# Kernel optimization log

Hardware: AMD Instinct MI355X
Metric: run time of the kernel (lower is better)

## Reference

```python
import jax, jax.numpy as jnp
import numpy as np

S = 1024      # flattened hierarchical sequence length
D = 1024      # n_embd
H = 16        # n_head
HD = D // H   # head dim (64)
NL = 6        # n_layer
DFF = 4 * D
EPS = 1.1920929e-07  # torch rms_norm default eps (float32 machine eps)


def setup_inputs() -> dict:
    key = jax.random.key(0)
    ks = jax.random.split(key, 12)
    s = 0.02
    return {
        "x": jax.random.normal(ks[0], (1, S, D), jnp.float32),
        "Wq": jax.random.normal(ks[1], (NL, D, D), jnp.float32) * s,
        "Wk": jax.random.normal(ks[2], (NL, D, D), jnp.float32) * s,
        "Wv": jax.random.normal(ks[3], (NL, D, D), jnp.float32) * s,
        "Wo": jax.random.normal(ks[4], (NL, D, D), jnp.float32) * s,
        "lamb": jnp.full((NL,), 0.5, jnp.float32),
        "lambdas": jnp.tile(jnp.array([1.0, 0.0], jnp.float32), (NL, 1)),
        "Wfc": jax.random.normal(ks[5], (NL, DFF, D), jnp.float32) * s,
        "Wp": jax.random.normal(ks[6], (NL, D, DFF), jnp.float32) * s,
        "levels": jax.random.randint(ks[7], (S,), 0, 3, jnp.int32),
        "sample_idx": jnp.sort(jax.random.randint(ks[8], (S,), 0, 8, jnp.int32)),
    }


def rms(t):
    return t * jax.lax.rsqrt(jnp.mean(t * t, axis=-1, keepdims=True) + EPS)


def rope(t):
    # t: [B, T, H, hd]; torch-style half-split rotary
    hd = t.shape[-1]
    d = hd // 2
    inv = 1.0 / (10000.0 ** (jnp.arange(0, hd, 2, dtype=jnp.float32) / hd))
    fr = jnp.outer(jnp.arange(t.shape[1], dtype=jnp.float32), inv)  # [T, d]
    cos = jnp.cos(fr)[None, :, None, :]
    sin = jnp.sin(fr)[None, :, None, :]
    x1, x2 = t[..., :d], t[..., d:]
    return jnp.concatenate([x1 * cos + x2 * sin, -x1 * sin + x2 * cos], axis=-1)


def markov_mask(levels, sample_idx):
    # allowed(q,kv) = causal & same-sample & NOT(levels[kv]==0 and a level-0
    # token exists strictly between kv and q). Equivalent to the torch
    # markov_causal_mask, computed via a cumsum instead of torch.any.
    n = levels.shape[0]
    pos = jnp.arange(n)
    causal = pos[:, None] >= pos[None, :]
    same = sample_idx[:, None] == sample_idx[None, :]
    c = jnp.cumsum((levels == 0).astype(jnp.int32))
    cpad = jnp.concatenate([jnp.zeros((1,), jnp.int32), c])  # cpad[i]=#l0 in [0,i)
    # count of level-0 tokens at positions p with kv < p < q
    cnt = cpad[pos[:, None]] - cpad[pos[None, :] + 1]
    markov = (levels[None, :] == 0) & (cnt > 0)
    return causal & same & ~markov


def reference(x, Wq, Wk, Wv, Wo, lamb, lambdas, Wfc, Wp, levels, sample_idx):
    mask = markov_mask(levels, sample_idx)[None, None]  # [1,1,S,S]
    scale = HD ** -0.5
    neg = jnp.float32(-1e30)

    x = rms(x)          # norm of the hierarchical-trajectory embedding
    x0 = x
    v1 = None
    for i in range(NL):
        xl = lambdas[i, 0] * x + lambdas[i, 1] * x0
        xn = rms(xl)
        B, T = xn.shape[0], xn.shape[1]
        q = (xn @ Wq[i].T).reshape(B, T, H, HD)
        k = (xn @ Wk[i].T).reshape(B, T, H, HD)
        v = (xn @ Wv[i].T).reshape(B, T, H, HD)
        if v1 is None:
            v1 = v
        v = (1.0 - lamb[i]) * v + lamb[i] * v1   # value residual
        q, k = rms(q), rms(k)                    # QK RMSNorm
        q, k = rope(q), rope(k)
        scores = jnp.einsum("bqhd,bkhd->bhqk", q, k) * scale
        scores = jnp.where(mask, scores, neg)
        p = jax.nn.softmax(scores, axis=-1)
        y = jnp.einsum("bhqk,bkhd->bqhd", p, v).reshape(B, T, D)
        x = xl + y @ Wo[i].T
        h = rms(x) @ Wfc[i].T
        h = jnp.square(jax.nn.relu(h))           # relu(x)^2 activation
        x = x + h @ Wp[i].T
    return rms(x)
```

## Files before the change

kernel.cpp:

```cpp
#include <hip/hip_runtime.h>

#define SQ 1024
#define DM 1024
#define NH 16
#define HD 64
#define NL 6
#define DFF 4096
#define EPS 1.1920929e-07f

typedef __attribute__((ext_vector_type(8))) short short8;
typedef __attribute__((ext_vector_type(4))) float floatx4;
typedef __attribute__((address_space(1))) const unsigned int GU32;
typedef __attribute__((address_space(3))) unsigned int LU32;

__device__ __forceinline__ unsigned short f2b(float f) {
    union { float f; unsigned int u; } x; x.f = f;
    unsigned int r = x.u + 0x7fffu + ((x.u >> 16) & 1u);
    return (unsigned short)(r >> 16);
}

__device__ __forceinline__ float wsum(float v) {
#pragma unroll
    for (int m = 32; m >= 1; m >>= 1) v += __shfl_xor(v, m, 64);
    return v;
}
__device__ __forceinline__ float bsum(float v) {
    __shared__ float sh[4];
    v = wsum(v);
    __syncthreads();
    if ((threadIdx.x & 63) == 0) sh[threadIdx.x >> 6] = v;
    __syncthreads();
    return sh[0] + sh[1] + sh[2] + sh[3];
}

__global__ void convert_all(const float* __restrict__ s0, const float* __restrict__ s1,
                            const float* __restrict__ s2, const float* __restrict__ s3,
                            const float* __restrict__ s4, const float* __restrict__ s5,
                            unsigned short* __restrict__ d0, unsigned short* __restrict__ d1,
                            unsigned short* __restrict__ d2, unsigned short* __restrict__ d3,
                            unsigned short* __restrict__ d4, unsigned short* __restrict__ d5) {
    int bid = blockIdx.x;
    const float* src; unsigned short* dst; long base;
    if (bid < 1536)        { src = s0; dst = d0; base = (long)bid * 512; }
    else if (bid < 3072)   { src = s1; dst = d1; base = (long)(bid - 1536) * 512; }
    else if (bid < 4608)   { src = s2; dst = d2; base = (long)(bid - 3072) * 512; }
    else if (bid < 6144)   { src = s3; dst = d3; base = (long)(bid - 4608) * 512; }
    else if (bid < 12288)  { src = s4; dst = d4; base = (long)(bid - 6144) * 512; }
    else                   { src = s5; dst = d5; base = (long)(bid - 12288) * 512; }
    long i0 = base + threadIdx.x;
#pragma unroll
    for (int u = 0; u < 2; ++u) {
        long i = i0 + u * 256;
        float4 a = ((const float4*)src)[2 * i];
        float4 b = ((const float4*)src)[2 * i + 1];
        short8 o;
        o[0] = (short)f2b(a.x); o[1] = (short)f2b(a.y);
        o[2] = (short)f2b(a.z); o[3] = (short)f2b(a.w);
        o[4] = (short)f2b(b.x); o[5] = (short)f2b(b.y);
        o[6] = (short)f2b(b.z); o[7] = (short)f2b(b.w);
        *(short8*)(dst + i * 8) = o;
    }
}

__global__ void build_rope(float2* __restrict__ tab) {
    int i = blockIdx.x * 256 + threadIdx.x;
    int s = i >> 5, d = i & 31;
    float invf = expf(-((float)(2 * d) / (float)HD) * 9.210340371976184f);
    float fr = (float)s * invf;
    tab[i] = make_float2(cosf(fr), sinf(fr));
}

__global__ void scan_levels(const int* __restrict__ levels, int* __restrict__ cpad) {
    __shared__ int sh[SQ];
    int t = threadIdx.x;
    sh[t] = (levels[t] == 0) ? 1 : 0;
    __syncthreads();
    for (int off = 1; off < SQ; off <<= 1) {
        int v = (t >= off) ? sh[t - off] : 0;
        __syncthreads();
        sh[t] += v;
        __syncthreads();
    }
    cpad[t + 1] = sh[t];
    if (t == 0) cpad[0] = 0;
}

__global__ void build_mask_bits(const int* __restrict__ levels, const int* __restrict__ sidx,
                                const int* __restrict__ cpad, unsigned long long* __restrict__ mb) {
    int i = blockIdx.x * 256 + threadIdx.x;
    int q = i >> 10, k = i & 1023;
    bool causal = q >= k;
    bool same = sidx[q] == sidx[k];
    int cnt = cpad[q] - cpad[k + 1];
    bool markov = (levels[k] == 0) && (cnt > 0);
    bool pred = causal && same && !markov;
    unsigned long long bal = __ballot(pred);
    if ((threadIdx.x & 63) == 0) mb[(size_t)q * 16 + (k >> 6)] = bal;
}

__global__ void rms0(const float* __restrict__ xin, const float* __restrict__ lam2,
                     float* __restrict__ x0, float* __restrict__ xl,
                     unsigned short* __restrict__ xnb) {
    int row = blockIdx.x, t = threadIdx.x;
    float l0 = lam2[0], l1 = lam2[1];
    const float* rp = xin + (size_t)row * DM;
    float v[4]; float ss = 0.f;
#pragma unroll
    for (int j = 0; j < 4; ++j) { v[j] = rp[t + j * 256]; ss += v[j] * v[j]; }
    ss = bsum(ss);
    float inv = rsqrtf(ss / (float)DM + EPS);
    float coef = l0 + l1;
    float w[4]; float ss2 = 0.f;
#pragma unroll
    for (int j = 0; j < 4; ++j) {
        float r = v[j] * inv;
        x0[(size_t)row * DM + t + j * 256] = r;
        w[j] = coef * r;
        ss2 += w[j] * w[j];
    }
    ss2 = bsum(ss2);
    float inv2 = rsqrtf(ss2 / (float)DM + EPS);
#pragma unroll
    for (int j = 0; j < 4; ++j) {
        size_t idx = (size_t)row * DM + t + j * 256;
        xl[idx] = w[j];
        xnb[idx] = f2b(w[j] * inv2);
    }
}

__global__ __launch_bounds__(256, 2)
void gemm_qkv(const unsigned short* __restrict__ A,
              const unsigned short* __restrict__ B0,
              long long sB,
              unsigned short* __restrict__ qb, unsigned short* __restrict__ kb,
              float* __restrict__ v1, unsigned short* __restrict__ vt,
              const float2* __restrict__ rope,
              const float* __restrict__ lambp, int first) {
    constexpr int BM = 64, BN = 128, BK = 32;
    __shared__ unsigned short As[2][BM * BK];
    __shared__ unsigned short Bs[2][BN * BK];
    __shared__ unsigned short vtile[128 * 72];
    int t = threadIdx.x, wave = t >> 6, lane = t & 63;
    int m0 = blockIdx.y * BM, n0 = blockIdx.x * BN;
    int z = blockIdx.z;
    const unsigned short* Bb = B0 + (size_t)z * sB;
    int r = lane & 15, q4 = lane >> 4;
    int sr = lane >> 2, sseg = lane & 3;
    int wmo = (wave >> 1) * 32, wno = (wave & 1) * 64;

    floatx4 acc[2][4] = {};

    {
        const unsigned short* g = A + (size_t)(m0 + wave * 16 + sr) * DM + sseg * 8;
        __builtin_amdgcn_global_load_lds((GU32*)g, (LU32*)(&As[0][wave * 512]), 16, 0, 0);
    }
#pragma unroll
    for (int j = 0; j < 2; ++j) {
        int c = wave * 2 + j;
        const unsigned short* g = Bb + (size_t)(n0 + c * 16 + sr) * DM + sseg * 8;
        __builtin_amdgcn_global_load_lds((GU32*)g, (LU32*)(&Bs[0][c * 512]), 16, 0, 0);
    }
    __syncthreads();

    int cur = 0;
    for (int k0 = 0; k0 < DM; k0 += BK) {
        int kn = k0 + BK;
        if (kn < DM) {
            {
                const unsigned short* g = A + (size_t)(m0 + wave * 16 + sr) * DM + kn + sseg * 8;
                __builtin_amdgcn_global_load_lds((GU32*)g, (LU32*)(&As[cur ^ 1][wave * 512]), 16, 0, 0);
            }
#pragma unroll
            for (int j = 0; j < 2; ++j) {
                int c = wave * 2 + j;
                const unsigned short* g = Bb + (size_t)(n0 + c * 16 + sr) * DM + kn + sseg * 8;
                __builtin_amdgcn_global_load_lds((GU32*)g, (LU32*)(&Bs[cur ^ 1][c * 512]), 16, 0, 0);
            }
        }
        short8 af[2], bfr[4];
#pragma unroll
        for (int mi = 0; mi < 2; ++mi)
            af[mi] = *(const short8*)(&As[cur][(wmo + mi * 16 + r) * BK + q4 * 8]);
#pragma unroll
        for (int ni = 0; ni < 4; ++ni)
            bfr[ni] = *(const short8*)(&Bs[cur][(wno + ni * 16 + r) * BK + q4 * 8]);
#pragma unroll
        for (int mi = 0; mi < 2; ++mi)
#pragma unroll
            for (int ni = 0; ni < 4; ++ni)
                acc[mi][ni] = __builtin_amdgcn_mfma_f32_16x16x32_bf16(af[mi], bfr[ni], acc[mi][ni], 0, 0, 0);
        __syncthreads();
        cur ^= 1;
    }

    if (z == 2) {
        float l = lambp[0];
#pragma unroll
        for (int mi = 0; mi < 2; ++mi)
#pragma unroll
            for (int ni = 0; ni < 4; ++ni)
#pragma unroll
                for (int j = 0; j < 4; ++j) {
                    int row = m0 + wmo + mi * 16 + q4 * 4 + j;
                    int col = n0 + wno + ni * 16 + r;
                    float val = acc[mi][ni][j];
                    size_t gi = (size_t)row * DM + col;
                    float v1v;
                    if (first) { v1[gi] = val; v1v = val; } else v1v = v1[gi];
                    vtile[(col - n0) * 72 + (row - m0)] = f2b((1.f - l) * val + l * v1v);
                }
        __syncthreads();
#pragma unroll
        for (int jj = 0; jj < 4; ++jj) {
            int idx = jj * 256 + t;
            int cr = idx >> 3;
            int seg = idx & 7;
            short8 o = *(const short8*)(&vtile[cr * 72 + seg * 8]);
            *(short8*)(vt + (size_t)(n0 + cr) * SQ + m0 + seg * 8) = o;
        }
        return;
    }

    unsigned short* dst = z ? kb : qb;
#pragma unroll
    for (int mi = 0; mi < 2; ++mi) {
#pragma unroll
        for (int j = 0; j < 4; ++j) {
            int row = m0 + wmo + mi * 16 + q4 * 4 + j;
            float v0 = acc[mi][0][j], v1x = acc[mi][1][j], v2 = acc[mi][2][j], v3 = acc[mi][3][j];
            float ss = v0 * v0 + v1x * v1x + v2 * v2 + v3 * v3;
#pragma unroll
            for (int d = 1; d < 16; d <<= 1) ss += __shfl_xor(ss, d, 64);
            float inv = rsqrtf(ss * (1.f / 64.f) + EPS);
            v0 *= inv; v1x *= inv; v2 *= inv; v3 *= inv;
            float2 t0 = rope[row * 32 + r];
            float2 t1 = rope[row * 32 + 16 + r];
            size_t rb = (size_t)row * DM + n0 + wno + r;
            dst[rb]      = f2b(v0 * t0.x + v2 * t0.y);
            dst[rb + 16] = f2b(v1x * t1.x + v3 * t1.y);
            dst[rb + 32] = f2b(v2 * t0.x - v0 * t0.y);
            dst[rb + 48] = f2b(v3 * t1.x - v1x * t1.y);
        }
    }
}

__global__ __launch_bounds__(64)
void flash_attn(const unsigned short* __restrict__ qb, const unsigned short* __restrict__ kb,
                const unsigned short* __restrict__ vt, const unsigned long long* __restrict__ mb,
                unsigned short* __restrict__ yb) {
    __shared__ unsigned short Ps[16 * 64];
    int lane = threadIdx.x;
    int qt = blockIdx.x & 63, h = blockIdx.x >> 6;
    int q0 = qt * 16;
    int r = lane & 15, q4 = lane >> 4;
    const unsigned short* qp = qb + (size_t)(q0 + r) * DM + h * HD + q4 * 8;
    short8 aq0 = *(const short8*)qp;
    short8 aq1 = *(const short8*)(qp + 32);
    floatx4 o[4] = {};
    float m[4] = {-1e30f, -1e30f, -1e30f, -1e30f};
    float l[4] = {0.f, 0.f, 0.f, 0.f};
    int nk = (qt >> 2) + 1;
    for (int kt = 0; kt < nk; ++kt) {
        int k0 = kt * 64;
        unsigned long long mw[4];
#pragma unroll
        for (int j = 0; j < 4; ++j) mw[j] = mb[(size_t)(q0 + q4 * 4 + j) * 16 + kt];
        unsigned long long any = mw[0] | mw[1] | mw[2] | mw[3];
        if (__ballot(any != 0ull) == 0ull) continue;
        short8 bk[4][2], bv[4][2];
#pragma unroll
        for (int ni = 0; ni < 4; ++ni) {
            const unsigned short* kp = kb + (size_t)(k0 + ni * 16 + r) * DM + h * HD + q4 * 8;
            bk[ni][0] = *(const short8*)kp;
            bk[ni][1] = *(const short8*)(kp + 32);
            const unsigned short* vp = vt + (size_t)(h * HD + ni * 16 + r) * SQ + k0 + q4 * 8;
            bv[ni][0] = *(const short8*)vp;
            bv[ni][1] = *(const short8*)(vp + 32);
        }
        float sm[4][4];
#pragma unroll
        for (int ni = 0; ni < 4; ++ni) {
            floatx4 z = {};
            z = __builtin_amdgcn_mfma_f32_16x16x32_bf16(aq0, bk[ni][0], z, 0, 0, 0);
            z = __builtin_amdgcn_mfma_f32_16x16x32_bf16(aq1, bk[ni][1], z, 0, 0, 0);
#pragma unroll
            for (int j = 0; j < 4; ++j) {
                float sv = z[j] * 0.125f;
                bool bit = (mw[j] >> (ni * 16 + r)) & 1ull;
                sm[ni][j] = bit ? sv : -__builtin_inff();
            }
        }
        float alpha[4];
#pragma unroll
        for (int j = 0; j < 4; ++j) {
            float v = fmaxf(fmaxf(sm[0][j], sm[1][j]), fmaxf(sm[2][j], sm[3][j]));
#pragma unroll
            for (int d = 1; d < 16; d <<= 1) v = fmaxf(v, __shfl_xor(v, d, 64));
            float mn = fmaxf(m[j], v);
            alpha[j] = __expf(m[j] - mn);
            m[j] = mn;
        }
        float p[4][4];
        float rs[4] = {0.f, 0.f, 0.f, 0.f};
#pragma unroll
        for (int ni = 0; ni < 4; ++ni)
#pragma unroll
            for (int j = 0; j < 4; ++j) {
                p[ni][j] = __expf(sm[ni][j] - m[j]);
                rs[j] += p[ni][j];
            }
#pragma unroll
        for (int j = 0; j < 4; ++j) {
            float v = rs[j];
#pragma unroll
            for (int d = 1; d < 16; d <<= 1) v += __shfl_xor(v, d, 64);
            l[j] = l[j] * alpha[j] + v;
        }
#pragma unroll
        for (int ni = 0; ni < 4; ++ni)
#pragma unroll
            for (int j = 0; j < 4; ++j) {
                o[ni][j] *= alpha[j];
                Ps[(q4 * 4 + j) * 64 + ni * 16 + r] = f2b(p[ni][j]);
            }
        short8 ap0 = *(const short8*)(Ps + r * 64 + q4 * 8);
        short8 ap1 = *(const short8*)(Ps + r * 64 + 32 + q4 * 8);
#pragma unroll
        for (int ni = 0; ni < 4; ++ni) {
            o[ni] = __builtin_amdgcn_mfma_f32_16x16x32_bf16(ap0, bv[ni][0], o[ni], 0, 0, 0);
            o[ni] = __builtin_amdgcn_mfma_f32_16x16x32_bf16(ap1, bv[ni][1], o[ni], 0, 0, 0);
        }
    }
#pragma unroll
    for (int j = 0; j < 4; ++j) l[j] = 1.f / l[j];
#pragma unroll
    for (int ni = 0; ni < 4; ++ni)
#pragma unroll
        for (int j = 0; j < 4; ++j)
            yb[(size_t)(q0 + q4 * 4 + j) * DM + h * HD + ni * 16 + r] = f2b(o[ni][j] * l[j]);
}

template<int BM, int BN>
__global__ __launch_bounds__(256, 2)
void gemm_t(const unsigned short* __restrict__ A, int lda, long long sA,
            const unsigned short* __restrict__ B, int ldb, long long sB,
            float* Cf, unsigned short* Cb, int ldc, long long sC,
            const float* __restrict__ addsrc, int ldadd,
            int K, float scale, int act) {
    constexpr int BK = 32;
    constexpr int MI = BM / 32, NI = BN / 32;
    constexpr int CAW = BM / 64, CBW = BN / 64;
    __shared__ unsigned short As[2][BM * BK];
    __shared__ unsigned short Bs[2][BN * BK];

    int t = threadIdx.x;
    int wave = t >> 6, lane = t & 63;
    int m0 = blockIdx.y * BM, n0 = blockIdx.x * BN;
    int z = blockIdx.z;
    const unsigned short* Ab = A + (size_t)z * sA;
    const unsigned short* Bb = B + (size_t)z * sB;

    int r = lane & 15, q4 = lane >> 4;
    int sr = lane >> 2, sseg = lane & 3;
    int wmo = (wave >> 1) * (BM / 2);
    int wno = (wave & 1) * (BN / 2);

    floatx4 acc[MI][NI] = {};

#pragma unroll
    for (int j = 0; j < CAW; ++j) {
        int c = wave * CAW + j;
        const unsigned short* g = Ab + (size_t)(m0 + c * 16 + sr) * lda + sseg * 8;
        __builtin_amdgcn_global_load_lds((GU32*)g, (LU32*)(&As[0][c * 512]), 16, 0, 0);
    }
#pragma unroll
    for (int j = 0; j < CBW; ++j) {
        int c = wave * CBW + j;
        const unsigned short* g = Bb + (size_t)(n0 + c * 16 + sr) * ldb + sseg * 8;
        __builtin_amdgcn_global_load_lds((GU32*)g, (LU32*)(&Bs[0][c * 512]), 16, 0, 0);
    }
    __syncthreads();

    int cur = 0;
    for (int k0 = 0; k0 < K; k0 += BK) {
        int kn = k0 + BK;
        if (kn < K) {
#pragma unroll
            for (int j = 0; j < CAW; ++j) {
                int c = wave * CAW + j;
                const unsigned short* g = Ab + (size_t)(m0 + c * 16 + sr) * lda + kn + sseg * 8;
                __builtin_amdgcn_global_load_lds((GU32*)g, (LU32*)(&As[cur ^ 1][c * 512]), 16, 0, 0);
            }
#pragma unroll
            for (int j = 0; j < CBW; ++j) {
                int c = wave * CBW + j;
                const unsigned short* g = Bb + (size_t)(n0 + c * 16 + sr) * ldb + kn + sseg * 8;
                __builtin_amdgcn_global_load_lds((GU32*)g, (LU32*)(&Bs[cur ^ 1][c * 512]), 16, 0, 0);
            }
        }
        short8 af[MI], bfr[NI];
#pragma unroll
        for (int mi = 0; mi < MI; ++mi)
            af[mi] = *(const short8*)(&As[cur][(wmo + mi * 16 + r) * BK + q4 * 8]);
#pragma unroll
        for (int ni = 0; ni < NI; ++ni)
            bfr[ni] = *(const short8*)(&Bs[cur][(wno + ni * 16 + r) * BK + q4 * 8]);
#pragma unroll
        for (int mi = 0; mi < MI; ++mi)
#pragma unroll
            for (int ni = 0; ni < NI; ++ni)
                acc[mi][ni] = __builtin_amdgcn_mfma_f32_16x16x32_bf16(af[mi], bfr[ni], acc[mi][ni], 0, 0, 0);
        __syncthreads();
        cur ^= 1;
    }

    size_t cz = (size_t)z * sC;
#pragma unroll
    for (int mi = 0; mi < MI; ++mi) {
#pragma unroll
        for (int ni = 0; ni < NI; ++ni) {
            int col = n0 + wno + ni * 16 + r;
#pragma unroll
            for (int j = 0; j < 4; ++j) {
                int row = m0 + wmo + mi * 16 + q4 * 4 + j;
                float v = acc[mi][ni][j] * scale;
                if (addsrc) v += addsrc[(size_t)row * ldadd + col];
                if (act == 1) { v = fmaxf(v, 0.f); v = v * v; }
                if (Cf) Cf[cz + (size_t)row * ldc + col] = v;
                if (Cb) Cb[cz + (size_t)row * ldc + col] = f2b(v);
            }
        }
    }
}

__global__ void wo_rms(const float* __restrict__ xl, const float* __restrict__ pp,
                       float* __restrict__ x, unsigned short* __restrict__ xhb) {
    int row = blockIdx.x, t = threadIdx.x;
    const long n = (long)SQ * DM;
    size_t base = (size_t)row * DM;
    float a[4]; float ss = 0.f;
#pragma unroll
    for (int j = 0; j < 4; ++j) {
        size_t idx = base + t + j * 256;
        float v = xl[idx] + pp[idx] + pp[idx + n];
        x[idx] = v;
        a[j] = v; ss += v * v;
    }
    ss = bsum(ss);
    float inv = rsqrtf(ss / (float)DM + EPS);
#pragma unroll
    for (int j = 0; j < 4; ++j)
        xhb[base + t + j * 256] = f2b(a[j] * inv);
}

__global__ void proj_reduce_xlrms(const float* __restrict__ x, const float* __restrict__ pp,
                                  const float* __restrict__ x0, const float* __restrict__ lam2,
                                  float* __restrict__ xl, unsigned short* __restrict__ xnb,
                                  float* __restrict__ out, int last) {
    int row = blockIdx.x, t = threadIdx.x;
    const long n = (long)SQ * DM;
    size_t base = (size_t)row * DM;
    float l0 = 0.f, l1 = 0.f;
    if (!last) { l0 = lam2[0]; l1 = lam2[1]; }
    float a[4]; float ss = 0.f;
#pragma unroll
    for (int j = 0; j < 4; ++j) {
        size_t idx = base + t + j * 256;
        float v = x[idx] + pp[idx] + pp[idx + n] + pp[idx + 2 * n] + pp[idx + 3 * n];
        if (!last) { v = l0 * v + l1 * x0[idx]; xl[idx] = v; }
        a[j] = v; ss += v * v;
    }
    ss = bsum(ss);
    float inv = rsqrtf(ss / (float)DM + EPS);
#pragma unroll
    for (int j = 0; j < 4; ++j) {
        size_t idx = base + t + j * 256;
        if (last) out[idx] = a[j] * inv;
        else xnb[idx] = f2b(a[j] * inv);
    }
}

extern "C" void kernel_launch(void* const* d_in, const int* in_sizes, int n_in,
                              void* d_out, int out_size, void* d_ws, size_t ws_size,
                              hipStream_t stream) {
    const float* x_in    = (const float*)d_in[0];
    const float* Wq      = (const float*)d_in[1];
    const float* Wk      = (const float*)d_in[2];
    const float* Wv      = (const float*)d_in[3];
    const float* Wo      = (const float*)d_in[4];
    const float* lamb    = (const float*)d_in[5];
    const float* lambdas = (const float*)d_in[6];
    const float* Wfc     = (const float*)d_in[7];
    const float* Wp      = (const float*)d_in[8];
    const int*   levels  = (const int*)d_in[9];
    const int*   sidx    = (const int*)d_in[10];
    float* out = (float*)d_out;

    char* ws = (char*)d_ws;
    size_t off = 0;
    auto alloc = [&](size_t b) { void* p = ws + off; off = (off + b + 255) & ~(size_t)255; return p; };

    unsigned short* wq_b  = (unsigned short*)alloc((size_t)NL * DM * DM * 2);
    unsigned short* wk_b  = (unsigned short*)alloc((size_t)NL * DM * DM * 2);
    unsigned short* wv_b  = (unsigned short*)alloc((size_t)NL * DM * DM * 2);
    unsigned short* wo_b  = (unsigned short*)alloc((size_t)NL * DM * DM * 2);
    unsigned short* wfc_b = (unsigned short*)alloc((size_t)NL * DFF * DM * 2);
    unsigned short* wp_b  = (unsigned short*)alloc((size_t)NL * DM * DFF * 2);
    int* cpad             = (int*)alloc((SQ + 1) * 4);
    unsigned long long* mb = (unsigned long long*)alloc((size_t)SQ * 16 * 8);
    float2* rope          = (float2*)alloc((size_t)SQ * 32 * 8);
    float* x    = (float*)alloc((size_t)SQ * DM * 4);
    float* x0   = (float*)alloc((size_t)SQ * DM * 4);
    float* xl   = (float*)alloc((size_t)SQ * DM * 4);
    float* v1   = (float*)alloc((size_t)SQ * DM * 4);
    float* pp   = (float*)alloc((size_t)4 * SQ * DM * 4);
    unsigned short* xn_b = (unsigned short*)alloc((size_t)SQ * DM * 2);
    unsigned short* qb   = (unsigned short*)alloc((size_t)SQ * DM * 2);
    unsigned short* kb   = (unsigned short*)alloc((size_t)SQ * DM * 2);
    unsigned short* vt   = (unsigned short*)alloc((size_t)SQ * DM * 2);
    unsigned short* y_b  = (unsigned short*)alloc((size_t)SQ * DM * 2);
    unsigned short* xh_b = (unsigned short*)alloc((size_t)SQ * DM * 2);
    unsigned short* h_b  = (unsigned short*)alloc((size_t)SQ * DFF * 2);

    if (off > ws_size) return;

    const long long WSTRIDE = (long long)NL * DM * DM;
    const long long XSTRIDE = (long long)SQ * DM;

    convert_all<<<18432, 256, 0, stream>>>(Wq, Wk, Wv, Wo, Wfc, Wp,
                                           wq_b, wk_b, wv_b, wo_b, wfc_b, wp_b);

    scan_levels<<<1, 1024, 0, stream>>>(levels, cpad);
    build_mask_bits<<<4096, 256, 0, stream>>>(levels, sidx, cpad, mb);
    build_rope<<<128, 256, 0, stream>>>(rope);

    rms0<<<SQ, 256, 0, stream>>>(x_in, lambdas, x0, xl, xn_b);

    for (int i = 0; i < NL; ++i) {
        gemm_qkv<<<dim3(8, 16, 3), 256, 0, stream>>>(
            xn_b, wq_b + (size_t)i * DM * DM, WSTRIDE, qb, kb, v1, vt, rope,
            lamb + i, (i == 0) ? 1 : 0);

        flash_attn<<<1024, 64, 0, stream>>>(qb, kb, vt, mb, y_b);

        gemm_t<64, 64><<<dim3(16, 16, 2), 256, 0, stream>>>(
            y_b, DM, 512, wo_b + (size_t)i * DM * DM, DM, 512,
            pp, nullptr, DM, XSTRIDE, nullptr, 0, 512, 1.f, 0);
        wo_rms<<<SQ, 256, 0, stream>>>(xl, pp, x, xh_b);

        gemm_t<128, 64><<<dim3(64, 8, 1), 256, 0, stream>>>(
            xh_b, DM, 0, wfc_b + (size_t)i * DFF * DM, DM, 0,
            nullptr, h_b, DFF, 0, nullptr, 0, DM, 1.f, 1);
        gemm_t<128, 64><<<dim3(16, 8, 4), 256, 0, stream>>>(
            h_b, DFF, 1024, wp_b + (size_t)i * DM * DFF, DFF, 1024,
            pp, nullptr, DM, XSTRIDE, nullptr, 0, 1024, 1.f, 0);
        proj_reduce_xlrms<<<SQ, 256, 0, stream>>>(
            x, pp, x0, (i < NL - 1) ? (lambdas + 2 * (i + 1)) : nullptr,
            xl, xn_b, out, (i == NL - 1) ? 1 : 0);
    }
}
```

Baseline: 1.061 ms.

## Replace double-buffered BK=32 GEMM loops with single-buffered BK=64 tiles

Both the QKV GEMM and the generic templated GEMM drop the LDS double buffer and its prefetch of the next K tile. They now load a BK=64 tile into a single buffer, synchronise, and run two 32-wide MFMA sub-steps before the next sync. This halves the number of loop iterations and barriers per K. The cost is that global-to-LDS loads no longer overlap with MFMA compute, and the row stride of 64 bf16 in LDS may cause bank conflicts on the fragment reads.

```diff
diff --git a/kernel.cpp b/kernel.cpp
--- a/kernel.cpp
+++ b/kernel.cpp
@@ -136,61 +136,50 @@
               float* __restrict__ v1, unsigned short* __restrict__ vt,
               const float2* __restrict__ rope,
               const float* __restrict__ lambp, int first) {
-    constexpr int BM = 64, BN = 128, BK = 32;
-    __shared__ unsigned short As[2][BM * BK];
-    __shared__ unsigned short Bs[2][BN * BK];
+    constexpr int BM = 64, BN = 128, BK = 64;
+    __shared__ unsigned short As[BM * BK];
+    __shared__ unsigned short Bs[BN * BK];
     __shared__ unsigned short vtile[128 * 72];
     int t = threadIdx.x, wave = t >> 6, lane = t & 63;
     int m0 = blockIdx.y * BM, n0 = blockIdx.x * BN;
     int z = blockIdx.z;
     const unsigned short* Bb = B0 + (size_t)z * sB;
     int r = lane & 15, q4 = lane >> 4;
-    int sr = lane >> 2, sseg = lane & 3;
+    int sr8 = lane >> 3, sseg8 = lane & 7;
     int wmo = (wave >> 1) * 32, wno = (wave & 1) * 64;
 
     floatx4 acc[2][4] = {};
 
-    {
-        const unsigned short* g = A + (size_t)(m0 + wave * 16 + sr) * DM + sseg * 8;
-        __builtin_amdgcn_global_load_lds((GU32*)g, (LU32*)(&As[0][wave * 512]), 16, 0, 0);
-    }
-#pragma unroll
-    for (int j = 0; j < 2; ++j) {
-        int c = wave * 2 + j;
-        const unsigned short* g = Bb + (size_t)(n0 + c * 16 + sr) * DM + sseg * 8;
-        __builtin_amdgcn_global_load_lds((GU32*)g, (LU32*)(&Bs[0][c * 512]), 16, 0, 0);
-    }
-    __syncthreads();
-
-    int cur = 0;
     for (int k0 = 0; k0 < DM; k0 += BK) {
-        int kn = k0 + BK;
-        if (kn < DM) {
-            {
-                const unsigned short* g = A + (size_t)(m0 + wave * 16 + sr) * DM + kn + sseg * 8;
-                __builtin_amdgcn_global_load_lds((GU32*)g, (LU32*)(&As[cur ^ 1][wave * 512]), 16, 0, 0);
-            }
-#pragma unroll
-            for (int j = 0; j < 2; ++j) {
-                int c = wave * 2 + j;
-                const unsigned short* g = Bb + (size_t)(n0 + c * 16 + sr) * DM + kn + sseg * 8;
-                __builtin_amdgcn_global_load_lds((GU32*)g, (LU32*)(&Bs[cur ^ 1][c * 512]), 16, 0, 0);
-            }
-        }
-        short8 af[2], bfr[4];
-#pragma unroll
-        for (int mi = 0; mi < 2; ++mi)
-            af[mi] = *(const short8*)(&As[cur][(wmo + mi * 16 + r) * BK + q4 * 8]);
-#pragma unroll
-        for (int ni = 0; ni < 4; ++ni)
-            bfr[ni] = *(const short8*)(&Bs[cur][(wno + ni * 16 + r) * BK + q4 * 8]);
-#pragma unroll
-        for (int mi = 0; mi < 2; ++mi)
+#pragma unroll
+        for (int j = 0; j < 2; ++j) {
+            int c = wave * 2 + j;
+            const unsigned short* g = A + (size_t)(m0 + c * 8 + sr8) * DM + k0 + sseg8 * 8;
+            __builtin_amdgcn_global_load_lds((GU32*)g, (LU32*)(As + c * 512), 16, 0, 0);
+        }
+#pragma unroll
+        for (int j = 0; j < 4; ++j) {
+            int c = wave * 4 + j;
+            const unsigned short* g = Bb + (size_t)(n0 + c * 8 + sr8) * DM + k0 + sseg8 * 8;
+            __builtin_amdgcn_global_load_lds((GU32*)g, (LU32*)(Bs + c * 512), 16, 0, 0);
+        }
+        __syncthreads();
+#pragma unroll
+        for (int kk = 0; kk < 2; ++kk) {
+            short8 af[2], bfr[4];
+#pragma unroll
+            for (int mi = 0; mi < 2; ++mi)
+                af[mi] = *(const short8*)(As + (wmo + mi * 16 + r) * BK + kk * 32 + q4 * 8);
 #pragma unroll
             for (int ni = 0; ni < 4; ++ni)
-                acc[mi][ni] = __builtin_amdgcn_mfma_f32_16x16x32_bf16(af[mi], bfr[ni], acc[mi][ni], 0, 0, 0);
-        __syncthreads();
-        cur ^= 1;
+                bfr[ni] = *(const short8*)(Bs + (wno + ni * 16 + r) * BK + kk * 32 + q4 * 8);
+#pragma unroll
+            for (int mi = 0; mi < 2; ++mi)
+#pragma unroll
+                for (int ni = 0; ni < 4; ++ni)
+                    acc[mi][ni] = __builtin_amdgcn_mfma_f32_16x16x32_bf16(af[mi], bfr[ni], acc[mi][ni], 0, 0, 0);
+        }
+        __syncthreads();
     }
 
     if (z == 2) {
@@ -347,11 +336,11 @@
             float* Cf, unsigned short* Cb, int ldc, long long sC,
             const float* __restrict__ addsrc, int ldadd,
             int K, float scale, int act) {
-    constexpr int BK = 32;
+    constexpr int BK = 64;
     constexpr int MI = BM / 32, NI = BN / 32;
-    constexpr int CAW = BM / 64, CBW = BN / 64;
-    __shared__ unsigned short As[2][BM * BK];
-    __shared__ unsigned short Bs[2][BN * BK];
+    constexpr int CAW = BM / 32, CBW = BN / 32;
+    __shared__ unsigned short As[BM * BK];
+    __shared__ unsigned short Bs[BN * BK];
 
     int t = threadIdx.x;
     int wave = t >> 6, lane = t & 63;
@@ -361,57 +350,42 @@
     const unsigned short* Bb = B + (size_t)z * sB;
 
     int r = lane & 15, q4 = lane >> 4;
-    int sr = lane >> 2, sseg = lane & 3;
+    int sr8 = lane >> 3, sseg8 = lane & 7;
     int wmo = (wave >> 1) * (BM / 2);
     int wno = (wave & 1) * (BN / 2);
 
     floatx4 acc[MI][NI] = {};
 
-#pragma unroll
-    for (int j = 0; j < CAW; ++j) {
-        int c = wave * CAW + j;
-        const unsigned short* g = Ab + (size_t)(m0 + c * 16 + sr) * lda + sseg * 8;
-        __builtin_amdgcn_global_load_lds((GU32*)g, (LU32*)(&As[0][c * 512]), 16, 0, 0);
-    }
-#pragma unroll
-    for (int j = 0; j < CBW; ++j) {
-        int c = wave * CBW + j;
-        const unsigned short* g = Bb + (size_t)(n0 + c * 16 + sr) * ldb + sseg * 8;
-        __builtin_amdgcn_global_load_lds((GU32*)g, (LU32*)(&Bs[0][c * 512]), 16, 0, 0);
-    }
-    __syncthreads();
-
-    int cur = 0;
     for (int k0 = 0; k0 < K; k0 += BK) {
-        int kn = k0 + BK;
-        if (kn < K) {
-#pragma unroll
-            for (int j = 0; j < CAW; ++j) {
-                int c = wave * CAW + j;
-                const unsigned short* g = Ab + (size_t)(m0 + c * 16 + sr) * lda + kn + sseg * 8;
-                __builtin_amdgcn_global_load_lds((GU32*)g, (LU32*)(&As[cur ^ 1][c * 512]), 16, 0, 0);
-            }
-#pragma unroll
-            for (int j = 0; j < CBW; ++j) {
-                int c = wave * CBW + j;
-                const unsigned short* g = Bb + (size_t)(n0 + c * 16 + sr) * ldb + kn + sseg * 8;
-                __builtin_amdgcn_global_load_lds((GU32*)g, (LU32*)(&Bs[cur ^ 1][c * 512]), 16, 0, 0);
-            }
-        }
-        short8 af[MI], bfr[NI];
-#pragma unroll
-        for (int mi = 0; mi < MI; ++mi)
-            af[mi] = *(const short8*)(&As[cur][(wmo + mi * 16 + r) * BK + q4 * 8]);
-#pragma unroll
-        for (int ni = 0; ni < NI; ++ni)
-            bfr[ni] = *(const short8*)(&Bs[cur][(wno + ni * 16 + r) * BK + q4 * 8]);
-#pragma unroll
-        for (int mi = 0; mi < MI; ++mi)
+#pragma unroll
+        for (int j = 0; j < CAW; ++j) {
+            int c = wave * CAW + j;
+            const unsigned short* g = Ab + (size_t)(m0 + c * 8 + sr8) * lda + k0 + sseg8 * 8;
+            __builtin_amdgcn_global_load_lds((GU32*)g, (LU32*)(As + c * 512), 16, 0, 0);
+        }
+#pragma unroll
+        for (int j = 0; j < CBW; ++j) {
+            int c = wave * CBW + j;
+            const unsigned short* g = Bb + (size_t)(n0 + c * 8 + sr8) * ldb + k0 + sseg8 * 8;
+            __builtin_amdgcn_global_load_lds((GU32*)g, (LU32*)(Bs + c * 512), 16, 0, 0);
+        }
+        __syncthreads();
+#pragma unroll
+        for (int kk = 0; kk < 2; ++kk) {
+            short8 af[MI], bfr[NI];
+#pragma unroll
+            for (int mi = 0; mi < MI; ++mi)
+                af[mi] = *(const short8*)(As + (wmo + mi * 16 + r) * BK + kk * 32 + q4 * 8);
 #pragma unroll
             for (int ni = 0; ni < NI; ++ni)
-                acc[mi][ni] = __builtin_amdgcn_mfma_f32_16x16x32_bf16(af[mi], bfr[ni], acc[mi][ni], 0, 0, 0);
-        __syncthreads();
-        cur ^= 1;
+                bfr[ni] = *(const short8*)(Bs + (wno + ni * 16 + r) * BK + kk * 32 + q4 * 8);
+#pragma unroll
+            for (int mi = 0; mi < MI; ++mi)
+#pragma unroll
+                for (int ni = 0; ni < NI; ++ni)
+                    acc[mi][ni] = __builtin_amdgcn_mfma_f32_16x16x32_bf16(af[mi], bfr[ni], acc[mi][ni], 0, 0, 0);
+        }
+        __syncthreads();
     }
 
     size_t cz = (size_t)z * sC;
```

New measurement: 1.007 ms. -5.1%, faster.
